# Kernel optimization log

Measured on AMD Instinct MI355X. Metric: run time of the kernel, lower is better.

## Reference

```python
import jax, jax.numpy as jnp
import numpy as np

NUM_FIELDS = 26

def setup_inputs() -> dict:
    key = jax.random.key(0)
    ks = jax.random.split(key, 8)
    B, F, D, V, d, af = 4096, NUM_FIELDS, 13, 100000, 64, 64
    return {
        "sparse_feat": jax.random.randint(ks[0], (B, F), 0, V, dtype=jnp.int32),
        "dense_feat": jax.random.uniform(ks[1], (B, D), dtype=jnp.float32),
        "embed_table": jax.random.normal(ks[2], (V, d), dtype=jnp.float32) * 0.05,
        "lin_table": jax.random.normal(ks[3], (V,), dtype=jnp.float32) * 0.05,
        "w_dense": jax.random.normal(ks[4], (D,), dtype=jnp.float32) * 0.1,
        "bias": jnp.zeros((1,), dtype=jnp.float32),
        "W1": jax.random.normal(ks[5], (d, af), dtype=jnp.float32) * (1.0 / np.sqrt(d)),
        "b1": jnp.zeros((af,), dtype=jnp.float32),
        "w2": jax.random.normal(ks[6], (af,), dtype=jnp.float32) * (1.0 / np.sqrt(af)),
        "p": jax.random.normal(ks[7], (d,), dtype=jnp.float32) * (1.0 / np.sqrt(d)),
    }

def reference(sparse_feat, dense_feat, embed_table, lin_table, w_dense, bias, W1, b1, w2, p):
    # Embedding lookup: [B, F, d]
    emb = embed_table[sparse_feat]
    # Linear part: per-field scalar weights + dense linear + bias -> [B]
    linear_out = lin_table[sparse_feat].sum(axis=1) + dense_feat @ w_dense + bias[0]
    # Pairwise interactions i<j (static indices): [B, P, d]
    i_idx, j_idx = np.triu_indices(NUM_FIELDS, k=1)
    att_x = emb[:, i_idx, :] * emb[:, j_idx, :]
    # Attention MLP: Linear(d, af) + ReLU + Linear(af, 1, no bias) -> [B, P]
    h = jax.nn.relu(jnp.einsum('bpd,da->bpa', att_x, W1) + b1)
    att_w = jnp.einsum('bpa,a->bp', h, w2)
    att_score = jax.nn.softmax(att_w, axis=1)
    # Softmax-weighted sum over pairs -> [B, d], then final projection p -> [B]
    att_out = jnp.einsum('bpd,bp->bd', att_x, att_score)
    fm_att_out = att_out @ p
    return linear_out + fm_att_out
```

## Files before the change

### kernel.cpp

```cpp
#include <hip/hip_runtime.h>
#include <math.h>


#define NF 26
#define NP 325
#define NPP 336
#define NMT 21
#define ED 64
#define AF 64
#define NDENSE 13
#define BLOCK 128
#define ESTRIDE 72

typedef __attribute__((ext_vector_type(8))) _Float16 half8;
typedef __attribute__((ext_vector_type(4))) float f32x4;

__device__ __forceinline__ half8 shfl_xor_h8(half8 v, int off) {
    union { half8 h; int i[4]; } u; u.h = v;
    #pragma unroll
    for (int k = 0; k < 4; ++k) u.i[k] = __shfl_xor(u.i[k], off, 64);
    return u.h;
}

__global__ void prep_kernel(const float* __restrict__ W1,
                            _Float16* __restrict__ w1t,
                            unsigned short* __restrict__ tab)
{
    int t = threadIdx.x;
    for (int idx = t; idx < ED * AF; idx += 256) {
        int d = idx >> 6, a = idx & 63;
        w1t[a * ED + d] = (_Float16)W1[idx];
    }
    if (t < NPP) {
        unsigned short v = 0;
        if (t < NP) {
            int rem = t, i = 0;
            while (rem >= NF - 1 - i) { rem -= NF - 1 - i; ++i; }
            v = (unsigned short)(i | ((i + 1 + rem) << 8));
        }
        tab[t] = v;
    }
}

__global__ __launch_bounds__(BLOCK, 4)
void afm_kernel(const int*   __restrict__ sparse,
                const float* __restrict__ dense,
                const float* __restrict__ etab,
                const float* __restrict__ ltab,
                const float* __restrict__ wdense,
                const float* __restrict__ bias,
                const float* __restrict__ b1,
                const float* __restrict__ w2,
                const float* __restrict__ proj,
                const _Float16* __restrict__ w1t,
                const unsigned short* __restrict__ tab,
                float*       __restrict__ out)
{
    const int t    = threadIdx.x;
    const int wave = t >> 6;
    const int lane = t & 63;
    const int qd   = lane >> 4;
    const int ln   = lane & 15;
    const int r    = blockIdx.x;

    __shared__ alignas(16) _Float16 emb[NF][ESTRIDE];
    __shared__ alignas(16) float    scores[NPP];
    __shared__ float pw[2];

    half8 bfr[4][2];
    #pragma unroll
    for (int nt = 0; nt < 4; ++nt)
        #pragma unroll
        for (int kh = 0; kh < 2; ++kh)
            bfr[nt][kh] = *(const half8*)(w1t + (nt * 16 + ln) * ED + kh * 32 + qd * 8);

    float4 b1v4[4], w2v4[4];
    #pragma unroll
    for (int nt = 0; nt < 4; ++nt) {
        b1v4[nt] = *(const float4*)(b1 + nt * 16 + qd * 4);
        w2v4[nt] = *(const float4*)(w2 + nt * 16 + qd * 4);
    }

    const int* __restrict__ srow = sparse + r * NF;
    for (int task = t; task < NF * 8; task += BLOCK) {
        int f = task >> 3, c = task & 7;
        const float* src = etab + (size_t)srow[f] * ED + c * 8;
        float4 v0 = *(const float4*)(src);
        float4 v1 = *(const float4*)(src + 4);
        half8 h = { (_Float16)v0.x, (_Float16)v0.y, (_Float16)v0.z, (_Float16)v0.w,
                    (_Float16)v1.x, (_Float16)v1.y, (_Float16)v1.z, (_Float16)v1.w };
        *(half8*)(&emb[f][c * 8]) = h;
    }

    float lin = 0.f;
    if (wave == 0) {
        if (lane < NF) {
            lin = ltab[srow[lane]];
        } else if (lane >= 32 && lane < 32 + NDENSE) {
            int k = lane - 32;
            lin = dense[r * NDENSE + k] * wdense[k];
        }
        #pragma unroll
        for (int off = 32; off >= 1; off >>= 1) lin += __shfl_xor(lin, off, 64);
        lin += bias[0];
    }

    __syncthreads();

    for (int mt = wave; mt < NMT; mt += 2) {
        const int p0 = mt * 16 + ln;
        const unsigned pp = tab[p0];
        const int fi = pp & 0xff, fj = pp >> 8;

        half8 x0 = *(const half8*)(&emb[fi][qd * 8])      * *(const half8*)(&emb[fj][qd * 8]);
        half8 x1 = *(const half8*)(&emb[fi][32 + qd * 8]) * *(const half8*)(&emb[fj][32 + qd * 8]);

        float lg = 0.f;
        #pragma unroll
        for (int nt = 0; nt < 4; ++nt) {
            f32x4 acc = { b1v4[nt].x, b1v4[nt].y, b1v4[nt].z, b1v4[nt].w };
            acc = __builtin_amdgcn_mfma_f32_16x16x32_f16(bfr[nt][0], x0, acc, 0, 0, 0);
            acc = __builtin_amdgcn_mfma_f32_16x16x32_f16(bfr[nt][1], x1, acc, 0, 0, 0);
            lg = fmaf(fmaxf(acc[0], 0.f), w2v4[nt].x, lg);
            lg = fmaf(fmaxf(acc[1], 0.f), w2v4[nt].y, lg);
            lg = fmaf(fmaxf(acc[2], 0.f), w2v4[nt].z, lg);
            lg = fmaf(fmaxf(acc[3], 0.f), w2v4[nt].w, lg);
        }
        lg += __shfl_xor(lg, 16, 64);
        lg += __shfl_xor(lg, 32, 64);
        if (qd == 0) scores[p0] = (p0 < NP) ? lg : -INFINITY;
    }

    __syncthreads();

    float4 v0 = *(const float4*)(&scores[lane * 4]);
    float4 v1 = make_float4(-INFINITY, -INFINITY, -INFINITY, -INFINITY);
    if (lane < NPP / 4 - 64) v1 = *(const float4*)(&scores[(lane + 64) * 4]);

    float m = fmaxf(fmaxf(fmaxf(v0.x, v0.y), fmaxf(v0.z, v0.w)),
                    fmaxf(fmaxf(v1.x, v1.y), fmaxf(v1.z, v1.w)));
    #pragma unroll
    for (int off = 32; off >= 1; off >>= 1) m = fmaxf(m, __shfl_xor(m, off, 64));
    float4 e0, e1;
    e0.x = __expf(v0.x - m); e0.y = __expf(v0.y - m);
    e0.z = __expf(v0.z - m); e0.w = __expf(v0.w - m);
    e1.x = __expf(v1.x - m); e1.y = __expf(v1.y - m);
    e1.z = __expf(v1.z - m); e1.w = __expf(v1.w - m);
    float esum = e0.x + e0.y + e0.z + e0.w + e1.x + e1.y + e1.z + e1.w;
    #pragma unroll
    for (int off = 32; off >= 1; off >>= 1) esum += __shfl_xor(esum, off, 64);
    const float rinv = 1.0f / esum;

    __syncthreads();
    if (wave == 0) {
        e0.x *= rinv; e0.y *= rinv; e0.z *= rinv; e0.w *= rinv;
        *(float4*)(&scores[lane * 4]) = e0;
    } else if (lane < NPP / 4 - 64) {
        e1.x *= rinv; e1.y *= rinv; e1.z *= rinv; e1.w *= rinv;
        *(float4*)(&scores[(lane + 64) * 4]) = e1;
    }

    __syncthreads();

    const int dg  = lane & 7;
    const int sub = (wave << 3) + (lane >> 3);
    half8 acc8 = { (_Float16)0.f, (_Float16)0.f, (_Float16)0.f, (_Float16)0.f,
                   (_Float16)0.f, (_Float16)0.f, (_Float16)0.f, (_Float16)0.f };
    for (int it = 0; it < NPP / 16; ++it) {
        const int p = it * 16 + sub;
        const float s = scores[p];
        const unsigned pp = tab[p];
        const int fi = pp & 0xff, fj = pp >> 8;
        const _Float16 sh = (_Float16)s;
        half8 sv = { sh, sh, sh, sh, sh, sh, sh, sh };
        half8 x = *(const half8*)(&emb[fi][dg * 8]) * *(const half8*)(&emb[fj][dg * 8]);
        acc8 += sv * x;
    }
    acc8 += shfl_xor_h8(acc8, 8);
    acc8 += shfl_xor_h8(acc8, 16);
    acc8 += shfl_xor_h8(acc8, 32);
    float4 pa = *(const float4*)(proj + dg * 8);
    float4 pb = *(const float4*)(proj + dg * 8 + 4);
    float part = (float)acc8[0] * pa.x + (float)acc8[1] * pa.y
               + (float)acc8[2] * pa.z + (float)acc8[3] * pa.w
               + (float)acc8[4] * pb.x + (float)acc8[5] * pb.y
               + (float)acc8[6] * pb.z + (float)acc8[7] * pb.w;
    #pragma unroll
    for (int off = 1; off <= 4; off <<= 1) part += __shfl_xor(part, off, 64);
    if (lane == 0) pw[wave] = part;

    __syncthreads();
    if (t == 0) out[r] = lin + pw[0] + pw[1];
}

extern "C" void kernel_launch(void* const* d_in, const int* in_sizes, int n_in,
                              void* d_out, int out_size, void* d_ws, size_t ws_size,
                              hipStream_t stream) {
    const int*   sparse = (const int*)  d_in[0];
    const float* dense  = (const float*)d_in[1];
    const float* etab   = (const float*)d_in[2];
    const float* ltab   = (const float*)d_in[3];
    const float* wdense = (const float*)d_in[4];
    const float* bias   = (const float*)d_in[5];
    const float* W1     = (const float*)d_in[6];
    const float* b1     = (const float*)d_in[7];
    const float* w2     = (const float*)d_in[8];
    const float* proj   = (const float*)d_in[9];
    float* outp = (float*)d_out;

    _Float16*       w1t = (_Float16*)d_ws;
    unsigned short* tab = (unsigned short*)((char*)d_ws + 8192);

    const int B = in_sizes[0] / NF;

    prep_kernel<<<dim3(1), dim3(256), 0, stream>>>(W1, w1t, tab);
    afm_kernel<<<dim3(B), dim3(BLOCK), 0, stream>>>(
        sparse, dense, etab, ltab, wdense, bias, b1, w2, proj, w1t, tab, outp);
    (void)n_in; (void)out_size; (void)ws_size;
}
```

Baseline: 125.5 us.

## Process one row per wave with online softmax fused into MFMA scoring loop

Each wavefront now owns one batch row, with four rows per 256-thread block, so all block-level __syncthreads barriers become wave-local syncs. Attention logits, softmax and the weighted pair sum are fused into a single pass using an online (running max and sum) softmax. Each lane accumulates its own pair contributions in fp16 registers, which removes the score buffer in shared memory and the second recompute pass over the pair products. Next-iteration embedding loads are prefetched, and the result is reduced across lanes at the end. The trade-offs are more serial work per wave and some precision risk from fp16 accumulation with repeated alpha rescaling.

```diff
diff --git a/kernel.cpp b/kernel.cpp
--- a/kernel.cpp
+++ b/kernel.cpp
@@ -4,22 +4,20 @@
 
 #define NF 26
 #define NP 325
-#define NPP 336
 #define NMT 21
 #define ED 64
 #define AF 64
 #define NDENSE 13
-#define BLOCK 128
+#define WPB 4
+#define BLOCK (WPB * 64)
 #define ESTRIDE 72
 
 typedef __attribute__((ext_vector_type(8))) _Float16 half8;
 typedef __attribute__((ext_vector_type(4))) float f32x4;
 
-__device__ __forceinline__ half8 shfl_xor_h8(half8 v, int off) {
-    union { half8 h; int i[4]; } u; u.h = v;
-    #pragma unroll
-    for (int k = 0; k < 4; ++k) u.i[k] = __shfl_xor(u.i[k], off, 64);
-    return u.h;
+__device__ __forceinline__ void wsync() {
+    __builtin_amdgcn_fence(__ATOMIC_ACQ_REL, "workgroup");
+    __builtin_amdgcn_wave_barrier();
 }
 
 __global__ void prep_kernel(const float* __restrict__ W1,
@@ -31,7 +29,7 @@
         int d = idx >> 6, a = idx & 63;
         w1t[a * ED + d] = (_Float16)W1[idx];
     }
-    if (t < NPP) {
+    if (t < NMT * 16) {
         unsigned short v = 0;
         if (t < NP) {
             int rem = t, i = 0;
@@ -54,18 +52,20 @@
                 const float* __restrict__ proj,
                 const _Float16* __restrict__ w1t,
                 const unsigned short* __restrict__ tab,
-                float*       __restrict__ out)
+                float*       __restrict__ out,
+                int B)
 {
     const int t    = threadIdx.x;
     const int wave = t >> 6;
     const int lane = t & 63;
     const int qd   = lane >> 4;
     const int ln   = lane & 15;
-    const int r    = blockIdx.x;
-
-    __shared__ alignas(16) _Float16 emb[NF][ESTRIDE];
-    __shared__ alignas(16) float    scores[NPP];
-    __shared__ float pw[2];
+
+    const int r = blockIdx.x * WPB + wave;
+    if (r >= B) return;
+
+    __shared__ alignas(16) _Float16 emb_all[WPB][NF][ESTRIDE];
+    _Float16 (* __restrict__ emb)[ESTRIDE] = emb_all[wave];
 
     half8 bfr[4][2];
     #pragma unroll
@@ -82,7 +82,7 @@
     }
 
     const int* __restrict__ srow = sparse + r * NF;
-    for (int task = t; task < NF * 8; task += BLOCK) {
+    for (int task = lane; task < NF * 8; task += 64) {
         int f = task >> 3, c = task & 7;
         const float* src = etab + (size_t)srow[f] * ED + c * 8;
         float4 v0 = *(const float4*)(src);
@@ -93,27 +93,42 @@
     }
 
     float lin = 0.f;
-    if (wave == 0) {
-        if (lane < NF) {
-            lin = ltab[srow[lane]];
-        } else if (lane >= 32 && lane < 32 + NDENSE) {
-            int k = lane - 32;
-            lin = dense[r * NDENSE + k] * wdense[k];
+    if (lane < NF) {
+        lin = ltab[srow[lane]];
+    } else if (lane >= 32 && lane < 32 + NDENSE) {
+        int k = lane - 32;
+        lin = dense[r * NDENSE + k] * wdense[k];
+    }
+    #pragma unroll
+    for (int off = 32; off >= 1; off >>= 1) lin += __shfl_xor(lin, off, 64);
+    lin += bias[0];
+
+    wsync();
+
+    float m = -INFINITY, l = 0.f;
+    half8 acc0 = { (_Float16)0.f, (_Float16)0.f, (_Float16)0.f, (_Float16)0.f,
+                   (_Float16)0.f, (_Float16)0.f, (_Float16)0.f, (_Float16)0.f };
+    half8 acc1 = acc0;
+
+    unsigned pp = tab[ln];
+    int fi = pp & 0xff, fj = pp >> 8;
+    half8 ei0 = *(const half8*)(&emb[fi][qd * 8]);
+    half8 ei1 = *(const half8*)(&emb[fi][32 + qd * 8]);
+    half8 ej0 = *(const half8*)(&emb[fj][qd * 8]);
+    half8 ej1 = *(const half8*)(&emb[fj][32 + qd * 8]);
+
+    for (int mt = 0; mt < NMT; ++mt) {
+        half8 x0 = ei0 * ej0;
+        half8 x1 = ei1 * ej1;
+
+        if (mt + 1 < NMT) {
+            unsigned np = tab[(mt + 1) * 16 + ln];
+            int nfi = np & 0xff, nfj = np >> 8;
+            ei0 = *(const half8*)(&emb[nfi][qd * 8]);
+            ei1 = *(const half8*)(&emb[nfi][32 + qd * 8]);
+            ej0 = *(const half8*)(&emb[nfj][qd * 8]);
+            ej1 = *(const half8*)(&emb[nfj][32 + qd * 8]);
         }
-        #pragma unroll
-        for (int off = 32; off >= 1; off >>= 1) lin += __shfl_xor(lin, off, 64);
-        lin += bias[0];
-    }
-
-    __syncthreads();
-
-    for (int mt = wave; mt < NMT; mt += 2) {
-        const int p0 = mt * 16 + ln;
-        const unsigned pp = tab[p0];
-        const int fi = pp & 0xff, fj = pp >> 8;
-
-        half8 x0 = *(const half8*)(&emb[fi][qd * 8])      * *(const half8*)(&emb[fj][qd * 8]);
-        half8 x1 = *(const half8*)(&emb[fi][32 + qd * 8]) * *(const half8*)(&emb[fj][32 + qd * 8]);
 
         float lg = 0.f;
         #pragma unroll
@@ -128,69 +143,47 @@
         }
         lg += __shfl_xor(lg, 16, 64);
         lg += __shfl_xor(lg, 32, 64);
-        if (qd == 0) scores[p0] = (p0 < NP) ? lg : -INFINITY;
-    }
-
-    __syncthreads();
-
-    float4 v0 = *(const float4*)(&scores[lane * 4]);
-    float4 v1 = make_float4(-INFINITY, -INFINITY, -INFINITY, -INFINITY);
-    if (lane < NPP / 4 - 64) v1 = *(const float4*)(&scores[(lane + 64) * 4]);
-
-    float m = fmaxf(fmaxf(fmaxf(v0.x, v0.y), fmaxf(v0.z, v0.w)),
-                    fmaxf(fmaxf(v1.x, v1.y), fmaxf(v1.z, v1.w)));
-    #pragma unroll
-    for (int off = 32; off >= 1; off >>= 1) m = fmaxf(m, __shfl_xor(m, off, 64));
-    float4 e0, e1;
-    e0.x = __expf(v0.x - m); e0.y = __expf(v0.y - m);
-    e0.z = __expf(v0.z - m); e0.w = __expf(v0.w - m);
-    e1.x = __expf(v1.x - m); e1.y = __expf(v1.y - m);
-    e1.z = __expf(v1.z - m); e1.w = __expf(v1.w - m);
-    float esum = e0.x + e0.y + e0.z + e0.w + e1.x + e1.y + e1.z + e1.w;
-    #pragma unroll
-    for (int off = 32; off >= 1; off >>= 1) esum += __shfl_xor(esum, off, 64);
-    const float rinv = 1.0f / esum;
-
-    __syncthreads();
-    if (wave == 0) {
-        e0.x *= rinv; e0.y *= rinv; e0.z *= rinv; e0.w *= rinv;
-        *(float4*)(&scores[lane * 4]) = e0;
-    } else if (lane < NPP / 4 - 64) {
-        e1.x *= rinv; e1.y *= rinv; e1.z *= rinv; e1.w *= rinv;
-        *(float4*)(&scores[(lane + 64) * 4]) = e1;
-    }
-
-    __syncthreads();
-
-    const int dg  = lane & 7;
-    const int sub = (wave << 3) + (lane >> 3);
-    half8 acc8 = { (_Float16)0.f, (_Float16)0.f, (_Float16)0.f, (_Float16)0.f,
-                   (_Float16)0.f, (_Float16)0.f, (_Float16)0.f, (_Float16)0.f };
-    for (int it = 0; it < NPP / 16; ++it) {
-        const int p = it * 16 + sub;
-        const float s = scores[p];
-        const unsigned pp = tab[p];
-        const int fi = pp & 0xff, fj = pp >> 8;
-        const _Float16 sh = (_Float16)s;
-        half8 sv = { sh, sh, sh, sh, sh, sh, sh, sh };
-        half8 x = *(const half8*)(&emb[fi][dg * 8]) * *(const half8*)(&emb[fj][dg * 8]);
-        acc8 += sv * x;
-    }
-    acc8 += shfl_xor_h8(acc8, 8);
-    acc8 += shfl_xor_h8(acc8, 16);
-    acc8 += shfl_xor_h8(acc8, 32);
-    float4 pa = *(const float4*)(proj + dg * 8);
-    float4 pb = *(const float4*)(proj + dg * 8 + 4);
-    float part = (float)acc8[0] * pa.x + (float)acc8[1] * pa.y
-               + (float)acc8[2] * pa.z + (float)acc8[3] * pa.w
-               + (float)acc8[4] * pb.x + (float)acc8[5] * pb.y
-               + (float)acc8[6] * pb.z + (float)acc8[7] * pb.w;
-    #pragma unroll
-    for (int off = 1; off <= 4; off <<= 1) part += __shfl_xor(part, off, 64);
-    if (lane == 0) pw[wave] = part;
-
-    __syncthreads();
-    if (t == 0) out[r] = lin + pw[0] + pw[1];
+
+        const int p0 = mt * 16 + ln;
+        if (p0 >= NP) lg = -INFINITY;
+
+        float mn    = fmaxf(m, lg);
+        float alpha = __expf(m - mn);
+        float e     = __expf(lg - mn);
+        l = l * alpha + e;
+        m = mn;
+        _Float16 ah = (_Float16)alpha, eh = (_Float16)e;
+        half8 a8 = { ah, ah, ah, ah, ah, ah, ah, ah };
+        half8 e8 = { eh, eh, eh, eh, eh, eh, eh, eh };
+        acc0 = acc0 * a8 + x0 * e8;
+        acc1 = acc1 * a8 + x1 * e8;
+    }
+
+    float mg = m;
+    #pragma unroll
+    for (int off = 1; off <= 8; off <<= 1) mg = fmaxf(mg, __shfl_xor(mg, off, 64));
+    const float fac = __expf(m - mg);
+    float lsum = l * fac;
+    #pragma unroll
+    for (int off = 1; off <= 8; off <<= 1) lsum += __shfl_xor(lsum, off, 64);
+
+    float4 pa = *(const float4*)(proj + qd * 8);
+    float4 pb = *(const float4*)(proj + qd * 8 + 4);
+    float4 pc = *(const float4*)(proj + 32 + qd * 8);
+    float4 pd = *(const float4*)(proj + 32 + qd * 8 + 4);
+    float rr = (float)acc0[0] * pa.x + (float)acc0[1] * pa.y
+             + (float)acc0[2] * pa.z + (float)acc0[3] * pa.w
+             + (float)acc0[4] * pb.x + (float)acc0[5] * pb.y
+             + (float)acc0[6] * pb.z + (float)acc0[7] * pb.w
+             + (float)acc1[0] * pc.x + (float)acc1[1] * pc.y
+             + (float)acc1[2] * pc.z + (float)acc1[3] * pc.w
+             + (float)acc1[4] * pd.x + (float)acc1[5] * pd.y
+             + (float)acc1[6] * pd.z + (float)acc1[7] * pd.w;
+    rr *= fac;
+    #pragma unroll
+    for (int off = 1; off <= 32; off <<= 1) rr += __shfl_xor(rr, off, 64);
+
+    if (lane == 0) out[r] = lin + rr / lsum;
 }
 
 extern "C" void kernel_launch(void* const* d_in, const int* in_sizes, int n_in,
@@ -214,7 +207,7 @@
     const int B = in_sizes[0] / NF;
 
     prep_kernel<<<dim3(1), dim3(256), 0, stream>>>(W1, w1t, tab);
-    afm_kernel<<<dim3(B), dim3(BLOCK), 0, stream>>>(
-        sparse, dense, etab, ltab, wdense, bias, b1, w2, proj, w1t, tab, outp);
+    afm_kernel<<<dim3((B + WPB - 1) / WPB), dim3(BLOCK), 0, stream>>>(
+        sparse, dense, etab, ltab, wdense, bias, b1, w2, proj, w1t, tab, outp, B);
     (void)n_in; (void)out_size; (void)ws_size;
 }
```

After: 116.2 us. -7.4%, faster.
